# Performance work log

Measured on AMD Instinct MI355X. Metric: run time of the kernel, lower is better.

## Reference

```python
import jax, jax.numpy as jnp
import numpy as np

EPS = 1e-5

def layernorm(x, g, b):
    mu = jnp.mean(x, axis=-1, keepdims=True)
    var = jnp.mean((x - mu) ** 2, axis=-1, keepdims=True)
    return (x - mu) * jax.lax.rsqrt(var + EPS) * g + b

def setup_inputs() -> dict:
    key = jax.random.key(0)
    B, T, C, H = 4, 2048, 1024, 16
    hs = C // H  # 64
    ks = jax.random.split(key, 16)
    s_in = 1.0 / np.sqrt(C)
    s_hid = 1.0 / np.sqrt(4 * C)
    return {
        "x":   jax.random.normal(ks[0], (B, T, C), jnp.float32),
        # per-head projections, stacked over heads: [H, C, hs]
        "Wq":  jax.random.normal(ks[1], (H, C, hs), jnp.float32) * s_in,
        "Wk":  jax.random.normal(ks[2], (H, C, hs), jnp.float32) * s_in,
        "Wv":  jax.random.normal(ks[3], (H, C, hs), jnp.float32) * s_in,
        # output projection [C, C] (concat of heads -> C)
        "Wo":  jax.random.normal(ks[4], (C, C), jnp.float32) * s_in,
        "bo":  jnp.zeros((C,), jnp.float32),
        # layernorm params
        "g1":  jnp.ones((C,), jnp.float32),
        "be1": jnp.zeros((C,), jnp.float32),
        "g2":  jnp.ones((C,), jnp.float32),
        "be2": jnp.zeros((C,), jnp.float32),
        # feed-forward: C -> 4C -> C
        "W1":  jax.random.normal(ks[5], (C, 4 * C), jnp.float32) * s_in,
        "b1":  jnp.zeros((4 * C,), jnp.float32),
        "W2":  jax.random.normal(ks[6], (4 * C, C), jnp.float32) * s_hid,
        "b2":  jnp.zeros((C,), jnp.float32),
    }

def reference(x, Wq, Wk, Wv, Wo, bo, g1, be1, g2, be2, W1, b1, W2, b2):
    B, T, C = x.shape
    H, _, hs = Wq.shape
    scale = hs ** -0.5

    # --- self-attention on ln1(x) ---
    xn = layernorm(x, g1, be1)
    q = jnp.einsum('btc,hcd->bhtd', xn, Wq)
    k = jnp.einsum('btc,hcd->bhtd', xn, Wk)
    v = jnp.einsum('btc,hcd->bhtd', xn, Wv)
    scores = jnp.einsum('bhtd,bhsd->bhts', q, k) * scale  # [B,H,T,T]
    causal = jnp.tril(jnp.ones((T, T), dtype=bool))
    scores = jnp.where(causal, scores, jnp.finfo(scores.dtype).min)
    wei = jax.nn.softmax(scores, axis=-1)
    out = jnp.einsum('bhts,bhsd->bhtd', wei, v)           # [B,H,T,hs]
    out = out.transpose(0, 2, 1, 3).reshape(B, T, H * hs)  # concat heads
    x = x + out @ Wo + bo

    # --- feed-forward on ln2(x) ---
    xn2 = layernorm(x, g2, be2)
    h = jax.nn.relu(xn2 @ W1 + b1)
    x = x + h @ W2 + b2
    return x
```

## Files before the change

kernel.cpp:

```cpp
#include <hip/hip_runtime.h>
#include <hip/hip_bf16.h>

typedef __hip_bfloat16 bf16;
typedef __attribute__((ext_vector_type(8))) short bf16x8;
typedef __attribute__((ext_vector_type(4))) short s16x4;
typedef __attribute__((ext_vector_type(4))) float f32x4;

__device__ __forceinline__ float b2f(bf16 v) { return __bfloat162float(v); }
__device__ __forceinline__ bf16  f2b(float v) { return __float2bfloat16(v); }
__device__ __forceinline__ float ldf(const bf16* p)  { return __bfloat162float(*p); }
__device__ __forceinline__ float ldf(const float* p) { return *p; }
__device__ __forceinline__ void  stf(bf16* p, float v)  { *p = __float2bfloat16(v); }
__device__ __forceinline__ void  stf(float* p, float v) { *p = v; }

__device__ __forceinline__ void ld4(const float* p, float* v) {
    float4 t = *(const float4*)p;
    v[0] = t.x; v[1] = t.y; v[2] = t.z; v[3] = t.w;
}
__device__ __forceinline__ void ld4(const bf16* p, float* v) {
    s16x4 t = *(const s16x4*)p;
#pragma unroll
    for (int j = 0; j < 4; ++j) { short s = t[j]; v[j] = b2f(*(bf16*)&s); }
}

__device__ __forceinline__ void load_lds16(const bf16* g, short* lds) {
    __builtin_amdgcn_global_load_lds(
        (const __attribute__((address_space(1))) unsigned int*)g,
        (__attribute__((address_space(3))) unsigned int*)lds, 16, 0, 0);
}

template<typename InT>
__global__ __launch_bounds__(256) void ln_kernel(const InT* __restrict__ x,
                                                 const float* __restrict__ g,
                                                 const float* __restrict__ b,
                                                 bf16* __restrict__ out)
{
    const int C = 1024;
    int row = blockIdx.x;
    int tid = threadIdx.x;
    const InT* xr = x + (size_t)row * C;

    float v[4];
    ld4(xr + tid * 4, v);
    float s = 0.f, s2 = 0.f;
#pragma unroll
    for (int i = 0; i < 4; ++i) { s += v[i]; s2 += v[i] * v[i]; }
#pragma unroll
    for (int off = 32; off > 0; off >>= 1) {
        s  += __shfl_down(s,  off, 64);
        s2 += __shfl_down(s2, off, 64);
    }
    __shared__ float red[8];
    int wave = tid >> 6;
    if ((tid & 63) == 0) { red[wave] = s; red[wave + 4] = s2; }
    __syncthreads();
    float ts  = red[0] + red[1] + red[2] + red[3];
    float ts2 = red[4] + red[5] + red[6] + red[7];
    float mu  = ts * (1.f / 1024.f);
    float var = ts2 * (1.f / 1024.f) - mu * mu;
    float rstd = rsqrtf(var + 1e-5f);

    float4 gg = *(const float4*)(g + tid * 4);
    float4 bb = *(const float4*)(b + tid * 4);
    float gj[4] = {gg.x, gg.y, gg.z, gg.w};
    float bj[4] = {bb.x, bb.y, bb.z, bb.w};
    s16x4 o4;
#pragma unroll
    for (int j = 0; j < 4; ++j) {
        bf16 ob = f2b((v[j] - mu) * rstd * gj[j] + bj[j]);
        o4[j] = *(short*)&ob;
    }
    *(s16x4*)(out + (size_t)row * C + tid * 4) = o4;
}

__global__ __launch_bounds__(256) void prep_weights(
    const float* __restrict__ Wq, const float* __restrict__ Wk,
    const float* __restrict__ Wv, const float* __restrict__ Wo,
    const float* __restrict__ W1, const float* __restrict__ W2,
    bf16* __restrict__ wqkvt, bf16* __restrict__ wot,
    bf16* __restrict__ w1t, bf16* __restrict__ w2t)
{
    __shared__ float t[32][33];
    int tx = threadIdx.x & 31, ty = threadIdx.x >> 5;
    int id = blockIdx.x;
    const float* in; bf16* out; int in_ld, out_ld, n0, k0;
    if (id < 3072) {
        const float* Ws[3] = {Wq, Wk, Wv};
        int m = id >> 10, r = id & 1023;
        int z = r >> 6, rt = r & 63;
        in = Ws[m] + z * 65536;
        out = wqkvt + (size_t)(m * 1024 + z * 64) * 1024;
        in_ld = 64; out_ld = 1024;
        n0 = (rt & 1) * 32; k0 = (rt >> 1) * 32;
    } else if (id < 4096) {
        int r = id - 3072;
        in = Wo; out = wot; in_ld = 1024; out_ld = 1024;
        n0 = (r & 31) * 32; k0 = (r >> 5) * 32;
    } else if (id < 8192) {
        int r = id - 4096;
        in = W1; out = w1t; in_ld = 4096; out_ld = 1024;
        n0 = (r & 127) * 32; k0 = (r >> 7) * 32;
    } else {
        int r = id - 8192;
        in = W2; out = w2t; in_ld = 1024; out_ld = 4096;
        n0 = (r & 31) * 32; k0 = (r >> 5) * 32;
    }
#pragma unroll
    for (int i = 0; i < 4; ++i)
        t[ty + i * 8][tx] = in[(size_t)(k0 + ty + i * 8) * in_ld + n0 + tx];
    __syncthreads();
#pragma unroll
    for (int i = 0; i < 4; ++i)
        out[(size_t)(n0 + ty + i * 8) * out_ld + k0 + tx] = f2b(t[tx][ty + i * 8]);
}

__global__ __launch_bounds__(256) void vt_kernel(
    const bf16* __restrict__ qkv, bf16* __restrict__ vt, int T)
{
    __shared__ float t[32][33];
    int tx = threadIdx.x & 31, ty = threadIdx.x >> 5;
    int z = blockIdx.z, b = z >> 4, h = z & 15;
    const bf16* in = qkv + (size_t)b * T * 3072 + 2048 + h * 64;
    bf16* out = vt + (size_t)z * 64 * T;
    int n0 = blockIdx.x * 32, k0 = blockIdx.y * 32;
#pragma unroll
    for (int i = 0; i < 4; ++i)
        t[ty + i * 8][tx] = b2f(in[(size_t)(k0 + ty + i * 8) * 3072 + n0 + tx]);
    __syncthreads();
#pragma unroll
    for (int i = 0; i < 4; ++i)
        out[(size_t)(n0 + ty + i * 8) * T + k0 + tx] = f2b(t[tx][ty + i * 8]);
}

template<int BK, bool RELU, bool HAS_BIAS, bool HAS_RES, typename ResT, typename OutT>
__global__ __launch_bounds__(256) void gemm_bt(
    const bf16* __restrict__ A, int lda,
    const bf16* __restrict__ Bt, int ldb,
    const float* __restrict__ bias,
    const ResT* __restrict__ res, int ldr,
    OutT* __restrict__ Cm, int ldc,
    int M, int N, int K)
{
    __shared__ short As[2][128 * BK];
    __shared__ short Bs[2][128 * BK];
    int tid = threadIdx.x, wv = tid >> 6, ln = tid & 63;

    int f = blockIdx.x + blockIdx.y * gridDim.x;
    int nby = gridDim.y;
    int by = f % nby, bx = f / nby;
    int bm0 = by * 128, bn0 = bx * 128;

    int wm = (wv & 1) * 64, wn = (wv >> 1) * 64;
    int quad = ln >> 4, lane15 = ln & 15;

    f32x4 acc[4][4] = {};

    const bf16* Ab = A + (size_t)bm0 * lda;
    const bf16* Bb = Bt + (size_t)bn0 * ldb;

    auto stage = [&](int buf, int kk) {
        if constexpr (BK == 32) {
            int srow = ln >> 2;
            int scol = (((ln & 3) ^ ((ln >> 3) & 3)) * 8);
#pragma unroll
            for (int i = 0; i < 2; ++i) {
                int ch = wv + i * 4;
                load_lds16(Ab + (size_t)(ch * 16 + srow) * lda + kk + scol,
                           &As[buf][ch * 16 * 32]);
                load_lds16(Bb + (size_t)(ch * 16 + srow) * ldb + kk + scol,
                           &Bs[buf][ch * 16 * 32]);
            }
        } else {
            int srow = ln >> 3;
            int scol = ((ln & 7) ^ srow) * 8;
#pragma unroll
            for (int i = 0; i < 4; ++i) {
                int r0 = i * 32 + wv * 8;
                load_lds16(Ab + (size_t)(r0 + srow) * lda + kk + scol,
                           &As[buf][r0 * 64]);
                load_lds16(Bb + (size_t)(r0 + srow) * ldb + kk + scol,
                           &Bs[buf][r0 * 64]);
            }
        }
    };

    stage(0, 0);
    __syncthreads();

    int cur = 0;
    for (int k0 = 0; k0 < K; k0 += BK) {
        if (k0 + BK < K) stage(cur ^ 1, k0 + BK);
        if constexpr (BK == 32) {
            int sw = (quad ^ ((lane15 >> 1) & 3)) * 8;
            bf16x8 af[4], bfr[4];
#pragma unroll
            for (int mi = 0; mi < 4; ++mi)
                af[mi] = *(const bf16x8*)&As[cur][(wm + mi * 16 + lane15) * 32 + sw];
#pragma unroll
            for (int ni = 0; ni < 4; ++ni)
                bfr[ni] = *(const bf16x8*)&Bs[cur][(wn + ni * 16 + lane15) * 32 + sw];
#pragma unroll
            for (int mi = 0; mi < 4; ++mi)
#pragma unroll
                for (int ni = 0; ni < 4; ++ni)
                    acc[mi][ni] = __builtin_amdgcn_mfma_f32_16x16x32_bf16(
                        af[mi], bfr[ni], acc[mi][ni], 0, 0, 0);
        } else {
#pragma unroll
            for (int ks = 0; ks < 2; ++ks) {
                int sw = (((ks * 4 + quad) ^ (lane15 & 7)) * 8);
                bf16x8 af[4], bfr[4];
#pragma unroll
                for (int mi = 0; mi < 4; ++mi)
                    af[mi] = *(const bf16x8*)&As[cur][(wm + mi * 16 + lane15) * 64 + sw];
#pragma unroll
                for (int ni = 0; ni < 4; ++ni)
                    bfr[ni] = *(const bf16x8*)&Bs[cur][(wn + ni * 16 + lane15) * 64 + sw];
#pragma unroll
                for (int mi = 0; mi < 4; ++mi)
#pragma unroll
                    for (int ni = 0; ni < 4; ++ni)
                        acc[mi][ni] = __builtin_amdgcn_mfma_f32_16x16x32_bf16(
                            af[mi], bfr[ni], acc[mi][ni], 0, 0, 0);
            }
        }
        __syncthreads();
        cur ^= 1;
    }

#pragma unroll
    for (int mi = 0; mi < 4; ++mi) {
#pragma unroll
        for (int r = 0; r < 4; ++r) {
            int gm = bm0 + wm + mi * 16 + quad * 4 + r;
#pragma unroll
            for (int ni = 0; ni < 4; ++ni) {
                int gn = bn0 + wn + ni * 16 + lane15;
                float v = acc[mi][ni][r];
                if (HAS_BIAS) v += bias[gn];
                if (HAS_RES)  v += ldf(res + (size_t)gm * ldr + gn);
                if (RELU)     v = fmaxf(v, 0.f);
                stf(Cm + (size_t)gm * ldc + gn, v);
            }
        }
    }
}

__device__ __forceinline__ void attn_tile_q(
    const short* __restrict__ Ks, const short* __restrict__ Vs,
    short* __restrict__ Psw,
    const bf16x8* qf, f32x4* oacc, float& mrun, float& lrun,
    int ktbase, int qmin, int quad, int lane15, int r7)
{
    const float scale2 = 0.18033688011112042f;
    const int PS = 72;
    f32x4 sacc[4] = {};
    __builtin_amdgcn_s_setprio(1);
#pragma unroll
    for (int ks = 0; ks < 2; ++ks) {
        int so = ((ks * 4 + quad) ^ r7) * 8;
#pragma unroll
        for (int mi = 0; mi < 4; ++mi) {
            bf16x8 kf = *(const bf16x8*)&Ks[(mi * 16 + lane15) * 64 + so];
            sacc[mi] = __builtin_amdgcn_mfma_f32_16x16x32_bf16(kf, qf[ks], sacc[mi], 0, 0, 0);
        }
    }
    __builtin_amdgcn_s_setprio(0);

    if (ktbase + 63 > qmin) {
        int ql = qmin + lane15;
#pragma unroll
        for (int mi = 0; mi < 4; ++mi)
#pragma unroll
            for (int r = 0; r < 4; ++r)
                if (ktbase + mi * 16 + quad * 4 + r > ql) sacc[mi][r] = -3e38f;
    }

    float mx = sacc[0][0];
#pragma unroll
    for (int mi = 0; mi < 4; ++mi)
#pragma unroll
        for (int r = 0; r < 4; ++r) mx = fmaxf(mx, sacc[mi][r]);
    mx = fmaxf(mx, __shfl_xor(mx, 16, 64));
    mx = fmaxf(mx, __shfl_xor(mx, 32, 64));
    float pmax = mx * scale2;

    if (!__all(pmax <= mrun + 11.5f)) {
        float mn = fmaxf(mrun, pmax);
        float alpha = exp2f(mrun - mn);
        mrun = mn;
        lrun *= alpha;
#pragma unroll
        for (int di = 0; di < 4; ++di)
#pragma unroll
            for (int r = 0; r < 4; ++r) oacc[di][r] *= alpha;
    }

    float psum = 0.f;
#pragma unroll
    for (int mi = 0; mi < 4; ++mi) {
        float p[4];
#pragma unroll
        for (int r = 0; r < 4; ++r) {
            p[r] = exp2f(fmaf(sacc[mi][r], scale2, -mrun));
            psum += p[r];
        }
        short tmp[4];
#pragma unroll
        for (int r = 0; r < 4; ++r) {
            bf16 pb = f2b(p[r]);
            tmp[r] = *(short*)&pb;
        }
        *(s16x4*)&Psw[lane15 * PS + mi * 16 + quad * 4] = *(s16x4*)tmp;
    }
    lrun += psum;

    __builtin_amdgcn_s_setprio(1);
#pragma unroll
    for (int ks = 0; ks < 2; ++ks) {
        int so = ((ks * 4 + quad) ^ r7) * 8;
        bf16x8 pf = *(const bf16x8*)&Psw[lane15 * PS + ks * 32 + quad * 8];
#pragma unroll
        for (int di = 0; di < 4; ++di) {
            bf16x8 vf = *(const bf16x8*)&Vs[(di * 16 + lane15) * 64 + so];
            oacc[di] = __builtin_amdgcn_mfma_f32_16x16x32_bf16(vf, pf, oacc[di], 0, 0, 0);
        }
    }
    __builtin_amdgcn_s_setprio(0);
}

__global__ __launch_bounds__(512, 4) void attn_kernel(
    const bf16* __restrict__ qkv, const bf16* __restrict__ vt,
    bf16* __restrict__ o, int T)
{
    const int LDQ = 3072;
    const int PS = 72;
    int bx = blockIdx.x;
    int qta = 15 - bx;
    int qtb = bx;
    int h = blockIdx.y, b = blockIdx.z;
    int tid = threadIdx.x, wv = tid >> 6, ln = tid & 63;
    int quad = ln >> 4, lane15 = ln & 15, r7 = lane15 & 7;

    __shared__ short KV[2][2][64 * 64];
    __shared__ short Ps[2][8][16 * PS];

    int lr = ln >> 3;
    int lc = ((ln & 7) ^ lr) * 8;

    const bf16* kbase = qkv + (size_t)(b * T) * LDQ + 1024 + h * 64;
    const bf16* vbase = vt + (size_t)((b * 16 + h) * 64) * T;

#pragma unroll
    for (int i = 0; i < 2; ++i) {
        int ch = wv * 2 + i;
        load_lds16(qkv + (size_t)(b * T + qta * 128 + ch * 8 + lr) * LDQ + h * 64 + lc,
                   &KV[0][0][ch * 512]);
        load_lds16(qkv + (size_t)(b * T + qtb * 128 + ch * 8 + lr) * LDQ + h * 64 + lc,
                   &KV[1][0][ch * 512]);
    }
    __syncthreads();
    bf16x8 qfa[2], qfb[2];
#pragma unroll
    for (int ks = 0; ks < 2; ++ks) {
        int off = (wv * 16 + lane15) * 64 + (((ks * 4 + quad) ^ r7) * 8);
        qfa[ks] = *(const bf16x8*)&KV[0][0][off];
        qfb[ks] = *(const bf16x8*)&KV[1][0][off];
    }
    __syncthreads();

    f32x4 oacca[4] = {}, oaccb[4] = {};
    float mra = -1e30f, lra = 0.f, mrb = -1e30f, lrb = 0.f;
    int qmina = qta * 128 + wv * 16;
    int qminb = qtb * 128 + wv * 16;
    int ntiles = 2 * qta + 2;

    load_lds16(kbase + (size_t)(wv * 8 + lr) * LDQ + lc, &KV[0][0][wv * 8 * 64]);
    load_lds16(vbase + (size_t)(wv * 8 + lr) * T + lc, &KV[0][1][wv * 8 * 64]);

    for (int kt = 0; kt < ntiles; ++kt) {
        __syncthreads();
        if (kt + 1 < ntiles) {
            int nb = (kt + 1) & 1;
            load_lds16(kbase + (size_t)((kt + 1) * 64 + wv * 8 + lr) * LDQ + lc,
                       &KV[nb][0][wv * 8 * 64]);
            load_lds16(vbase + (size_t)(wv * 8 + lr) * T + (kt + 1) * 64 + lc,
                       &KV[nb][1][wv * 8 * 64]);
        }
        const short* Ks = &KV[kt & 1][0][0];
        const short* Vs = &KV[kt & 1][1][0];
        int kb = kt * 64;

        if (kb <= qmina + 15)
            attn_tile_q(Ks, Vs, &Ps[0][wv][0], qfa, oacca, mra, lra,
                        kb, qmina, quad, lane15, r7);
        if (kb <= qminb + 15)
            attn_tile_q(Ks, Vs, &Ps[1][wv][0], qfb, oaccb, mrb, lrb,
                        kb, qminb, quad, lane15, r7);
    }

    lra += __shfl_xor(lra, 16, 64);
    lra += __shfl_xor(lra, 32, 64);
    float inva = 1.f / lra;
    size_t rowa = (size_t)(b * T + qta * 128 + wv * 16 + lane15);
#pragma unroll
    for (int di = 0; di < 4; ++di) {
        short tmp[4];
#pragma unroll
        for (int r = 0; r < 4; ++r) {
            bf16 ob = f2b(oacca[di][r] * inva);
            tmp[r] = *(short*)&ob;
        }
        *(s16x4*)&o[rowa * 1024 + h * 64 + di * 16 + quad * 4] = *(s16x4*)tmp;
    }

    lrb += __shfl_xor(lrb, 16, 64);
    lrb += __shfl_xor(lrb, 32, 64);
    float invb = 1.f / lrb;
    size_t rowb = (size_t)(b * T + qtb * 128 + wv * 16 + lane15);
#pragma unroll
    for (int di = 0; di < 4; ++di) {
        short tmp[4];
#pragma unroll
        for (int r = 0; r < 4; ++r) {
            bf16 ob = f2b(oaccb[di][r] * invb);
            tmp[r] = *(short*)&ob;
        }
        *(s16x4*)&o[rowb * 1024 + h * 64 + di * 16 + quad * 4] = *(s16x4*)tmp;
    }
}

extern "C" void kernel_launch(void* const* d_in, const int* in_sizes, int n_in,
                              void* d_out, int out_size, void* d_ws, size_t ws_size,
                              hipStream_t stream)
{
    (void)in_sizes; (void)n_in; (void)out_size; (void)ws_size;
    const float* x   = (const float*)d_in[0];
    const float* Wq  = (const float*)d_in[1];
    const float* Wk  = (const float*)d_in[2];
    const float* Wv  = (const float*)d_in[3];
    const float* Wo  = (const float*)d_in[4];
    const float* bo  = (const float*)d_in[5];
    const float* g1  = (const float*)d_in[6];
    const float* be1 = (const float*)d_in[7];
    const float* g2  = (const float*)d_in[8];
    const float* be2 = (const float*)d_in[9];
    const float* W1  = (const float*)d_in[10];
    const float* b1  = (const float*)d_in[11];
    const float* W2  = (const float*)d_in[12];
    const float* b2  = (const float*)d_in[13];

    const int T = 2048, M = 4 * T;
    const size_t MB = 1ull << 20;
    char* ws = (char*)d_ws;

    bf16*  xn    = (bf16*)(ws + 0 * MB);
    bf16*  qkv   = (bf16*)(ws + 16 * MB);
    bf16*  vt    = (bf16*)(ws + 64 * MB);
    bf16*  wqkvt = (bf16*)(ws + 80 * MB);
    bf16*  x1b   = (bf16*)(ws + 80 * MB);
    bf16*  wot   = (bf16*)(ws + 96 * MB);
    bf16*  xn2   = (bf16*)(ws + 96 * MB);
    bf16*  w1t   = (bf16*)(ws + 112 * MB);
    bf16*  w2t   = (bf16*)(ws + 120 * MB);
    bf16*  attnb = (bf16*)(ws + 0 * MB);
    bf16*  hb    = (bf16*)(ws + 0 * MB);

    dim3 blk(256);

    prep_weights<<<12288, blk, 0, stream>>>(Wq, Wk, Wv, Wo, W1, W2,
                                            wqkvt, wot, w1t, w2t);

    ln_kernel<float><<<M, blk, 0, stream>>>(x, g1, be1, xn);

    gemm_bt<32, false, false, false, float, bf16><<<dim3(24, 64), blk, 0, stream>>>(
        xn, 1024, wqkvt, 1024, nullptr, nullptr, 0, qkv, 3072, M, 3072, 1024);

    vt_kernel<<<dim3(2, T / 32, 64), blk, 0, stream>>>(qkv, vt, T);

    attn_kernel<<<dim3(8, 16, 4), dim3(512), 0, stream>>>(qkv, vt, attnb, T);

    gemm_bt<32, false, true, true, float, bf16><<<dim3(8, 64), blk, 0, stream>>>(
        attnb, 1024, wot, 1024, bo, x, 1024, x1b, 1024, M, 1024, 1024);

    ln_kernel<bf16><<<M, blk, 0, stream>>>(x1b, g2, be2, xn2);

    gemm_bt<32, true, true, false, float, bf16><<<dim3(32, 64), blk, 0, stream>>>(
        xn2, 1024, w1t, 1024, b1, nullptr, 0, hb, 4096, M, 4096, 1024);

    gemm_bt<64, false, true, true, bf16, float><<<dim3(8, 64), blk, 0, stream>>>(
        hb, 4096, w2t, 4096, b2, x1b, 1024, (float*)d_out, 1024, M, 1024, 4096);
}
```

Before: 488.3 us.

## Add 256x256 eight-wave pipelined GEMM for QKV and FFN1 projections

Introduces a new GEMM kernel with 256x256 output tiles, 8 waves per block, a 4-deep LDS ring filled by direct global-to-LDS loads, and split MFMA phases separated by barriers with priority raising. It also remaps blocks across XCD groups, and it replaces the 128x128 GEMM for the QKV projection and the first feed-forward layer. The goal is more data reuse per loaded tile and better overlap of memory loads with matrix math. In exchange it uses heavy register pressure (a 128-float accumulator per thread), a large LDS footprint, and hand-tuned vmcnt waits that must match the exact load count.

```diff
diff --git a/kernel.cpp b/kernel.cpp
--- a/kernel.cpp
+++ b/kernel.cpp
@@ -132,6 +132,116 @@
         out[(size_t)(n0 + ty + i * 8) * T + k0 + tx] = f2b(t[tx][ty + i * 8]);
 }
 
+template<bool RELU, bool HAS_BIAS, typename OutT>
+__global__ __launch_bounds__(512, 2) void gemm8p(
+    const bf16* __restrict__ A, int lda,
+    const bf16* __restrict__ Bt, int ldb,
+    const float* __restrict__ bias,
+    OutT* __restrict__ Cm, int ldc,
+    int M, int N, int K)
+{
+    __shared__ short As[4][8192];
+    __shared__ short Bs[4][8192];
+    int tid = threadIdx.x, wv = tid >> 6, ln = tid & 63;
+    int quad = ln >> 4, lane15 = ln & 15;
+
+    int nbn = N >> 8;
+    int nwg = gridDim.x;
+    int f2 = (blockIdx.x & 7) * (nwg >> 3) + (blockIdx.x >> 3);
+    int by = f2 / nbn, bx = f2 % nbn;
+    int bm0 = by << 8, bn0 = bx << 8;
+
+    int wr = wv >> 2, wc = wv & 3;
+    const int NT = K >> 5;
+
+    int sr = tid >> 2;
+    int sc = ((tid & 3) ^ ((sr >> 1) & 3)) * 8;
+    const bf16* Ab1 = A  + (size_t)(bm0 + sr) * lda + sc;
+    const bf16* Ab2 = A  + (size_t)(bm0 + 128 + sr) * lda + sc;
+    const bf16* Bb1 = Bt + (size_t)(bn0 + sr) * ldb + sc;
+    const bf16* Bb2 = Bt + (size_t)(bn0 + 128 + sr) * ldb + sc;
+
+#define STAGE_A8(bf_, u_) { \
+    load_lds16(Ab1 + (u_) * 32, &As[bf_][wv * 512]); \
+    load_lds16(Ab2 + (u_) * 32, &As[bf_][4096 + wv * 512]); }
+#define STAGE_B8(bf_, u_) { \
+    load_lds16(Bb1 + (u_) * 32, &Bs[bf_][wv * 512]); \
+    load_lds16(Bb2 + (u_) * 32, &Bs[bf_][4096 + wv * 512]); }
+
+    f32x4 acc[8][4] = {};
+    int arow = wr * 128 + lane15;
+    int brow = wc * 64 + lane15;
+    int sw = (quad ^ ((lane15 >> 1) & 3)) * 8;
+
+    STAGE_A8(0, 0); STAGE_B8(0, 0);
+    STAGE_A8(1, 1); STAGE_B8(1, 1);
+    STAGE_A8(2, 2); STAGE_B8(2, 2);
+    asm volatile("s_waitcnt vmcnt(8)" ::: "memory");
+    __builtin_amdgcn_s_barrier();
+
+    for (int t = 0; t < NT; ++t) {
+        int buf = t & 3;
+        const short* Al = &As[buf][0];
+        const short* Bl = &Bs[buf][0];
+
+        bf16x8 af[8];
+#pragma unroll
+        for (int mi = 0; mi < 8; ++mi)
+            af[mi] = *(const bf16x8*)&Al[(arow + mi * 16) * 32 + sw];
+        bf16x8 bf0 = *(const bf16x8*)&Bl[(brow +  0) * 32 + sw];
+        bf16x8 bf1 = *(const bf16x8*)&Bl[(brow + 16) * 32 + sw];
+        if (t + 3 < NT) STAGE_A8((t + 3) & 3, t + 3);
+        __builtin_amdgcn_s_barrier();
+        __builtin_amdgcn_s_setprio(1);
+#pragma unroll
+        for (int mi = 0; mi < 8; ++mi) {
+            acc[mi][0] = __builtin_amdgcn_mfma_f32_16x16x32_bf16(af[mi], bf0, acc[mi][0], 0, 0, 0);
+            acc[mi][1] = __builtin_amdgcn_mfma_f32_16x16x32_bf16(af[mi], bf1, acc[mi][1], 0, 0, 0);
+        }
+        __builtin_amdgcn_s_setprio(0);
+        __builtin_amdgcn_s_barrier();
+
+        bf16x8 bf2 = *(const bf16x8*)&Bl[(brow + 32) * 32 + sw];
+        bf16x8 bf3 = *(const bf16x8*)&Bl[(brow + 48) * 32 + sw];
+        if (t + 3 < NT) STAGE_B8((t + 3) & 3, t + 3);
+        if (t < NT - 3) {
+            asm volatile("s_waitcnt vmcnt(8)" ::: "memory");
+        } else if (t == NT - 3) {
+            asm volatile("s_waitcnt vmcnt(4)" ::: "memory");
+        } else if (t == NT - 2) {
+            asm volatile("s_waitcnt vmcnt(0)" ::: "memory");
+        }
+        __builtin_amdgcn_s_barrier();
+        __builtin_amdgcn_s_setprio(1);
+#pragma unroll
+        for (int mi = 0; mi < 8; ++mi) {
+            acc[mi][2] = __builtin_amdgcn_mfma_f32_16x16x32_bf16(af[mi], bf2, acc[mi][2], 0, 0, 0);
+            acc[mi][3] = __builtin_amdgcn_mfma_f32_16x16x32_bf16(af[mi], bf3, acc[mi][3], 0, 0, 0);
+        }
+        __builtin_amdgcn_s_setprio(0);
+        __builtin_amdgcn_s_barrier();
+    }
+
+#undef STAGE_A8
+#undef STAGE_B8
+
+#pragma unroll
+    for (int mi = 0; mi < 8; ++mi) {
+#pragma unroll
+        for (int r = 0; r < 4; ++r) {
+            int gm = bm0 + wr * 128 + mi * 16 + quad * 4 + r;
+#pragma unroll
+            for (int ni = 0; ni < 4; ++ni) {
+                int gn = bn0 + wc * 64 + ni * 16 + lane15;
+                float v = acc[mi][ni][r];
+                if (HAS_BIAS) v += bias[gn];
+                if (RELU)     v = fmaxf(v, 0.f);
+                stf(Cm + (size_t)gm * ldc + gn, v);
+            }
+        }
+    }
+}
+
 template<int BK, bool RELU, bool HAS_BIAS, bool HAS_RES, typename ResT, typename OutT>
 __global__ __launch_bounds__(256) void gemm_bt(
     const bf16* __restrict__ A, int lda,
@@ -473,8 +583,8 @@
 
     ln_kernel<float><<<M, blk, 0, stream>>>(x, g1, be1, xn);
 
-    gemm_bt<32, false, false, false, float, bf16><<<dim3(24, 64), blk, 0, stream>>>(
-        xn, 1024, wqkvt, 1024, nullptr, nullptr, 0, qkv, 3072, M, 3072, 1024);
+    gemm8p<false, false, bf16><<<dim3(384), dim3(512), 0, stream>>>(
+        xn, 1024, wqkvt, 1024, nullptr, qkv, 3072, M, 3072, 1024);
 
     vt_kernel<<<dim3(2, T / 32, 64), blk, 0, stream>>>(qkv, vt, T);
 
@@ -485,8 +595,8 @@
 
     ln_kernel<bf16><<<M, blk, 0, stream>>>(x1b, g2, be2, xn2);
 
-    gemm_bt<32, true, true, false, float, bf16><<<dim3(32, 64), blk, 0, stream>>>(
-        xn2, 1024, w1t, 1024, b1, nullptr, 0, hb, 4096, M, 4096, 1024);
+    gemm8p<true, true, bf16><<<dim3(512), dim3(512), 0, stream>>>(
+        xn2, 1024, w1t, 1024, b1, hb, 4096, M, 4096, 1024);
 
     gemm_bt<64, false, true, true, bf16, float><<<dim3(8, 64), blk, 0, stream>>>(
         hb, 4096, w2t, 4096, b2, x1b, 1024, (float*)d_out, 1024, M, 1024, 4096);
```

After: 495.3 us. About the same (+1.4%).
